# Kernel optimization log

Hardware: AMD Instinct MI355X
Metric: run time of the kernel (lower is better)

## Reference

```python
import jax, jax.numpy as jnp
import numpy as np

N_NODES = 50000
N_EDGES = 800000
NUM_FEATS = 128
HIDDEN = 256
NUM_GRAPHS = 512
BN_EPS = 1e-5


def setup_inputs() -> dict:
    key = jax.random.key(0)
    ks = jax.random.split(key, 12)
    x = jax.random.normal(ks[0], (N_NODES, NUM_FEATS), dtype=jnp.float32)
    edge_index = jax.random.randint(ks[1], (2, N_EDGES), 0, N_NODES, dtype=jnp.int64)
    batch = jnp.sort(jax.random.randint(ks[2], (N_NODES,), 0, NUM_GRAPHS, dtype=jnp.int64))
    s1 = 1.0 / np.sqrt(NUM_FEATS)
    s2 = 1.0 / np.sqrt(HIDDEN)
    return {
        "x": x,
        "edge_index": edge_index,
        "batch": batch,
        "w1a": jax.random.normal(ks[3], (NUM_FEATS, HIDDEN), dtype=jnp.float32) * s1,
        "b1a": jnp.zeros((HIDDEN,), jnp.float32),
        "w2a": jax.random.normal(ks[4], (HIDDEN, HIDDEN), dtype=jnp.float32) * s2,
        "b2a": jnp.zeros((HIDDEN,), jnp.float32),
        "ga": jnp.ones((HIDDEN,), jnp.float32),
        "ba": jnp.zeros((HIDDEN,), jnp.float32),
        "w1s": jax.random.normal(ks[5], (2, HIDDEN, HIDDEN), dtype=jnp.float32) * s2,
        "b1s": jnp.zeros((2, HIDDEN), jnp.float32),
        "w2s": jax.random.normal(ks[6], (2, HIDDEN, HIDDEN), dtype=jnp.float32) * s2,
        "b2s": jnp.zeros((2, HIDDEN), jnp.float32),
        "gs": jnp.ones((2, HIDDEN), jnp.float32),
        "bs": jnp.zeros((2, HIDDEN), jnp.float32),
    }


def _gin_layer(h, src, dst, w1, b1, w2, b2, gamma, beta):
    # GIN aggregation: (1 + eps=0) * x + sum over in-neighbors
    agg = jax.ops.segment_sum(h[src], dst, num_segments=N_NODES)
    z = h + agg
    z = jax.nn.relu(z @ w1 + b1)
    z = jax.nn.relu(z @ w2 + b2)
    # BatchNorm1d (training mode: biased batch statistics over nodes)
    mu = jnp.mean(z, axis=0)
    var = jnp.var(z, axis=0)
    return gamma * (z - mu) * jax.lax.rsqrt(var + BN_EPS) + beta


def reference(x, edge_index, batch, w1a, b1a, w2a, b2a, ga, ba,
              w1s, b1s, w2s, b2s, gs, bs):
    src, dst = edge_index[0], edge_index[1]
    h = _gin_layer(x, src, dst, w1a, b1a, w2a, b2a, ga, ba)
    for i in range(w1s.shape[0]):
        h = _gin_layer(h, src, dst, w1s[i], b1s[i], w2s[i], b2s[i], gs[i], bs[i])
    # global_mean_pool over graph ids
    sums = jax.ops.segment_sum(h, batch, num_segments=NUM_GRAPHS)
    counts = jax.ops.segment_sum(jnp.ones((h.shape[0],), h.dtype), batch,
                                 num_segments=NUM_GRAPHS)
    return sums / jnp.maximum(counts, 1.0)[:, None]
```

## Files before the change

kernel.cpp:

```cpp
#include <hip/hip_runtime.h>
#include <cstdint>
#include <cstddef>


constexpr int N_NODES  = 50000;
constexpr int N_EDGES  = 800000;
constexpr int F_IN     = 128;
constexpr int HID      = 256;
constexpr int N_GRAPHS = 512;
constexpr float BN_EPS = 1e-5f;

constexpr int SCAN_CHUNK = 4096;
constexpr int SCAN_NB    = (N_NODES + SCAN_CHUNK - 1) / SCAN_CHUNK;

typedef unsigned short u16;
typedef u16 u16x2 __attribute__((ext_vector_type(2)));
typedef u16 u16x4 __attribute__((ext_vector_type(4)));
typedef u16 u16x8 __attribute__((ext_vector_type(8)));
typedef __bf16 bf16x8 __attribute__((ext_vector_type(8)));
typedef float f32x4 __attribute__((ext_vector_type(4)));

__device__ __forceinline__ u16 f2bf(float f) {
    uint32_t u = __float_as_uint(f);
    uint32_t r = (u + 0x7FFFu + ((u >> 16) & 1u)) >> 16;
    return (u16)r;
}
__device__ __forceinline__ float bf2f(u16 h) {
    return __uint_as_float(((uint32_t)h) << 16);
}

__global__ void f2bf_k(const float* __restrict__ in, u16* __restrict__ outp, int n8) {
    int i = blockIdx.x * 256 + threadIdx.x;
    if (i >= n8) return;
    float4 a = reinterpret_cast<const float4*>(in)[i * 2];
    float4 b = reinterpret_cast<const float4*>(in)[i * 2 + 1];
    u16x8 v;
    v[0] = f2bf(a.x); v[1] = f2bf(a.y); v[2] = f2bf(a.z); v[3] = f2bf(a.w);
    v[4] = f2bf(b.x); v[5] = f2bf(b.y); v[6] = f2bf(b.z); v[7] = f2bf(b.w);
    reinterpret_cast<u16x8*>(outp)[i] = v;
}

__global__ void hist_k(const int* __restrict__ dst, int* __restrict__ deg) {
    int e = blockIdx.x * 256 + threadIdx.x;
    if (e < N_EDGES) atomicAdd(&deg[dst[e]], 1);
}

__global__ void scan_part1(const int* __restrict__ in, int* __restrict__ bsum) {
    __shared__ int sm[256];
    int t = threadIdx.x;
    int base = blockIdx.x * SCAN_CHUNK + t * 16;
    int s = 0;
#pragma unroll
    for (int j = 0; j < 16; j++) { int idx = base + j; s += (idx < N_NODES) ? in[idx] : 0; }
    sm[t] = s; __syncthreads();
    for (int off = 128; off > 0; off >>= 1) {
        if (t < off) sm[t] += sm[t + off];
        __syncthreads();
    }
    if (t == 0) bsum[blockIdx.x] = sm[0];
}

__global__ void scan_tops(int* __restrict__ bsum, int* __restrict__ rowptr) {
    if (threadIdx.x == 0 && blockIdx.x == 0) {
        int acc = 0;
        for (int i = 0; i < SCAN_NB; i++) { int v = bsum[i]; bsum[i] = acc; acc += v; }
        rowptr[N_NODES] = acc;
    }
}

__global__ void scan_final(const int* __restrict__ in, const int* __restrict__ bsum,
                           int* __restrict__ rowptr, int* __restrict__ cursor) {
    __shared__ int sm[256];
    int t = threadIdx.x;
    int base = blockIdx.x * SCAN_CHUNK + t * 16;
    int loc[16]; int s = 0;
#pragma unroll
    for (int j = 0; j < 16; j++) { int idx = base + j; loc[j] = s; s += (idx < N_NODES) ? in[idx] : 0; }
    sm[t] = s; __syncthreads();
    for (int off = 1; off < 256; off <<= 1) {
        int v = (t >= off) ? sm[t - off] : 0;
        __syncthreads();
        sm[t] += v;
        __syncthreads();
    }
    int excl = sm[t] - s + bsum[blockIdx.x];
#pragma unroll
    for (int j = 0; j < 16; j++) {
        int idx = base + j;
        if (idx < N_NODES) { int rp = excl + loc[j]; rowptr[idx] = rp; cursor[idx] = rp; }
    }
}

__global__ void build_csr(const int* __restrict__ src, const int* __restrict__ dst,
                          int* __restrict__ cursor, int* __restrict__ col) {
    int e = blockIdx.x * 256 + threadIdx.x;
    if (e < N_EDGES) {
        int d = dst[e];
        int p = atomicAdd(&cursor[d], 1);
        col[p] = src[e];
    }
}

template <int F, bool FOLD>
__global__ __launch_bounds__(256) void aggregate_k(const u16* __restrict__ h,
                                                   const int* __restrict__ rowptr,
                                                   const int* __restrict__ col,
                                                   const float* __restrict__ scsh,
                                                   u16* __restrict__ outp) {
    int node = blockIdx.x * 4 + (threadIdx.x >> 6);
    if (node >= N_NODES) return;
    int lane = threadIdx.x & 63;
    int beg = rowptr[node], end = rowptr[node + 1];
    if constexpr (F == 256) {
        const u16x4* hp = reinterpret_cast<const u16x4*>(h);
        u16x4 sv = hp[(size_t)node * 64 + lane];
        float acc[4] = {bf2f(sv[0]), bf2f(sv[1]), bf2f(sv[2]), bf2f(sv[3])};
        int e = beg;
        for (; e + 4 <= end; e += 4) {
            int s0 = col[e], s1 = col[e + 1], s2 = col[e + 2], s3 = col[e + 3];
            u16x4 v0 = hp[(size_t)s0 * 64 + lane];
            u16x4 v1 = hp[(size_t)s1 * 64 + lane];
            u16x4 v2 = hp[(size_t)s2 * 64 + lane];
            u16x4 v3 = hp[(size_t)s3 * 64 + lane];
#pragma unroll
            for (int i = 0; i < 4; i++)
                acc[i] += (bf2f(v0[i]) + bf2f(v1[i])) + (bf2f(v2[i]) + bf2f(v3[i]));
        }
        for (; e < end; ++e) {
            int s = col[e];
            u16x4 v = hp[(size_t)s * 64 + lane];
#pragma unroll
            for (int i = 0; i < 4; i++) acc[i] += bf2f(v[i]);
        }
        if constexpr (FOLD) {
            int c4 = lane * 4;
            float4 sc = *reinterpret_cast<const float4*>(&scsh[c4]);
            float4 sh = *reinterpret_cast<const float4*>(&scsh[HID + c4]);
            float m = (float)(end - beg + 1);
            acc[0] = acc[0] * sc.x + m * sh.x;
            acc[1] = acc[1] * sc.y + m * sh.y;
            acc[2] = acc[2] * sc.z + m * sh.z;
            acc[3] = acc[3] * sc.w + m * sh.w;
        }
        u16x4 r;
#pragma unroll
        for (int i = 0; i < 4; i++) r[i] = f2bf(acc[i]);
        reinterpret_cast<u16x4*>(outp)[(size_t)node * 64 + lane] = r;
    } else {
        const u16x2* hp = reinterpret_cast<const u16x2*>(h);
        u16x2 sv = hp[(size_t)node * 64 + lane];
        float acc[2] = {bf2f(sv[0]), bf2f(sv[1])};
        int e = beg;
        for (; e + 4 <= end; e += 4) {
            int s0 = col[e], s1 = col[e + 1], s2 = col[e + 2], s3 = col[e + 3];
            u16x2 v0 = hp[(size_t)s0 * 64 + lane];
            u16x2 v1 = hp[(size_t)s1 * 64 + lane];
            u16x2 v2 = hp[(size_t)s2 * 64 + lane];
            u16x2 v3 = hp[(size_t)s3 * 64 + lane];
#pragma unroll
            for (int i = 0; i < 2; i++)
                acc[i] += (bf2f(v0[i]) + bf2f(v1[i])) + (bf2f(v2[i]) + bf2f(v3[i]));
        }
        for (; e < end; ++e) {
            int s = col[e];
            u16x2 v = hp[(size_t)s * 64 + lane];
#pragma unroll
            for (int i = 0; i < 2; i++) acc[i] += bf2f(v[i]);
        }
        u16x2 r;
        r[0] = f2bf(acc[0]); r[1] = f2bf(acc[1]);
        reinterpret_cast<u16x2*>(outp)[(size_t)node * 64 + lane] = r;
    }
}

__global__ void wsplit_k(const float* __restrict__ W, u16* __restrict__ th,
                         u16* __restrict__ tl, int K) {
    int idx = blockIdx.x * 256 + threadIdx.x;
    int n = idx & 255, k = idx >> 8;
    float f = W[(size_t)k * 256 + n];
    u16 h = f2bf(f);
    th[(size_t)n * K + k] = h;
    tl[(size_t)n * K + k] = f2bf(f - bf2f(h));
}

template <int K, bool STATS>
__global__ __launch_bounds__(256, 2) void gemm_mfma(const u16* __restrict__ A,
                                                    const u16* __restrict__ Wth,
                                                    const u16* __restrict__ Wtl,
                                                    const float* __restrict__ bias,
                                                    u16* __restrict__ C,
                                                    float* __restrict__ stats) {
    constexpr int BM = 128, BK = 32;
    __shared__ alignas(16) u16 Ah[BM * BK];
    __shared__ alignas(16) u16 Bh[HID * BK];
    __shared__ alignas(16) u16 Bl[HID * BK];
    __shared__ float smsum[HID];
    __shared__ float smsq[HID];

    const int tid  = threadIdx.x;
    const int r0   = blockIdx.x * BM;
    const int lane = tid & 63, wid = tid >> 6;
    const int wm = wid >> 1, wn = wid & 1;
    const int l15 = lane & 15, kg = lane >> 4;

    const int arow = tid >> 1, ahalf = tid & 1;
    const bool avalid = (r0 + arow) < N_NODES;
    const u16* aptr = A + (size_t)(r0 + arow) * K + ahalf * 16;
    const u16* bhptr = Wth + (size_t)tid * K;
    const u16* blptr = Wtl + (size_t)tid * K;

    f32x4 acc[4][8];
#pragma unroll
    for (int i = 0; i < 4; i++)
#pragma unroll
        for (int j = 0; j < 8; j++) acc[i][j] = (f32x4){0.f, 0.f, 0.f, 0.f};

    for (int k0 = 0; k0 < K; k0 += BK) {
        u16x8 av[2];
        if (avalid) {
            av[0] = *reinterpret_cast<const u16x8*>(aptr + k0);
            av[1] = *reinterpret_cast<const u16x8*>(aptr + k0 + 8);
        } else {
            av[0] = (u16x8){0, 0, 0, 0, 0, 0, 0, 0};
            av[1] = av[0];
        }
#pragma unroll
        for (int j = 0; j < 2; j++) {
            int c = ahalf * 2 + j;
            int off = arow * 64 + ((c ^ ((arow >> 1) & 3)) << 4);
            *reinterpret_cast<u16x8*>((char*)Ah + off) = av[j];
        }
#pragma unroll
        for (int j = 0; j < 4; j++) {
            u16x8 v = *reinterpret_cast<const u16x8*>(bhptr + k0 + j * 8);
            int off = tid * 64 + ((j ^ ((tid >> 1) & 3)) << 4);
            *reinterpret_cast<u16x8*>((char*)Bh + off) = v;
        }
#pragma unroll
        for (int j = 0; j < 4; j++) {
            u16x8 v = *reinterpret_cast<const u16x8*>(blptr + k0 + j * 8);
            int off = tid * 64 + ((j ^ ((tid >> 1) & 3)) << 4);
            *reinterpret_cast<u16x8*>((char*)Bl + off) = v;
        }
        __syncthreads();
        bf16x8 ah[4];
#pragma unroll
        for (int mi = 0; mi < 4; mi++) {
            int r = wm * 64 + mi * 16 + l15;
            int off = r * 64 + ((kg ^ ((r >> 1) & 3)) << 4);
            ah[mi] = __builtin_bit_cast(bf16x8, *reinterpret_cast<const u16x8*>((const char*)Ah + off));
        }
#pragma unroll
        for (int ni = 0; ni < 8; ni++) {
            int n = wn * 128 + ni * 16 + l15;
            int off = n * 64 + ((kg ^ ((n >> 1) & 3)) << 4);
            bf16x8 bh = __builtin_bit_cast(bf16x8, *reinterpret_cast<const u16x8*>((const char*)Bh + off));
            bf16x8 bl = __builtin_bit_cast(bf16x8, *reinterpret_cast<const u16x8*>((const char*)Bl + off));
#pragma unroll
            for (int mi = 0; mi < 4; mi++) {
                acc[mi][ni] = __builtin_amdgcn_mfma_f32_16x16x32_bf16(ah[mi], bh, acc[mi][ni], 0, 0, 0);
                acc[mi][ni] = __builtin_amdgcn_mfma_f32_16x16x32_bf16(ah[mi], bl, acc[mi][ni], 0, 0, 0);
            }
        }
        __syncthreads();
    }
    if constexpr (STATS) {
        smsum[tid] = 0.f;
        smsq[tid]  = 0.f;
        __syncthreads();
    }
    float bv[8];
#pragma unroll
    for (int ni = 0; ni < 8; ni++) bv[ni] = bias[wn * 128 + ni * 16 + l15];
    float ps[8] = {}, pq[8] = {};
#pragma unroll
    for (int mi = 0; mi < 4; mi++) {
        int rowb = r0 + wm * 64 + mi * 16 + kg * 4;
#pragma unroll
        for (int rr = 0; rr < 4; rr++) {
            int row = rowb + rr;
            if (row < N_NODES) {
                u16* cp = C + (size_t)row * HID + wn * 128 + l15;
#pragma unroll
                for (int ni = 0; ni < 8; ni++) {
                    float v = fmaxf(acc[mi][ni][rr] + bv[ni], 0.f);
                    cp[ni * 16] = f2bf(v);
                    if constexpr (STATS) { ps[ni] += v; pq[ni] += v * v; }
                }
            }
        }
    }
    if constexpr (STATS) {
#pragma unroll
        for (int ni = 0; ni < 8; ni++) {
            int c = wn * 128 + ni * 16 + l15;
            atomicAdd(&smsum[c], ps[ni]);
            atomicAdd(&smsq[c], pq[ni]);
        }
        __syncthreads();
        atomicAdd(&stats[tid], smsum[tid]);
        atomicAdd(&stats[HID + tid], smsq[tid]);
    }
}

__global__ void bn_finalize(const float* __restrict__ stats, const float* __restrict__ gamma,
                            const float* __restrict__ beta, float* __restrict__ scsh) {
    int c = threadIdx.x;
    float mu  = stats[c] * (1.f / N_NODES);
    float var = stats[HID + c] * (1.f / N_NODES) - mu * mu;
    float g = gamma[c] * rsqrtf(var + BN_EPS);
    scsh[c] = g;
    scsh[HID + c] = beta[c] - mu * g;
}

__device__ __forceinline__ int lowerb(const int* a, int key) {
    int lo = 0, hi = N_NODES;
    while (lo < hi) { int mid = (lo + hi) >> 1; if (a[mid] < key) lo = mid + 1; else hi = mid; }
    return lo;
}

__global__ void pool_k(const u16* __restrict__ h, const int* __restrict__ batch,
                       const float* __restrict__ scsh, float* __restrict__ out) {
    __shared__ int bnd[2];
    int g = blockIdx.x;
    if (threadIdx.x == 0) bnd[0] = lowerb(batch, g);
    if (threadIdx.x == 1) bnd[1] = lowerb(batch, g + 1);
    __syncthreads();
    int lo = bnd[0], hi = bnd[1];
    int c = threadIdx.x;
    float s = 0.f;
    for (int r = lo; r < hi; ++r) s += bf2f(h[(size_t)r * HID + c]);
    int cnt = hi - lo;
    float v = (cnt > 0) ? (scsh[c] * (s / (float)cnt) + scsh[HID + c]) : 0.f;
    out[(size_t)g * HID + c] = v;
}

extern "C" void kernel_launch(void* const* d_in, const int* in_sizes, int n_in,
                              void* d_out, int out_size, void* d_ws, size_t ws_size,
                              hipStream_t stream) {
    const float* x   = (const float*)d_in[0];
    const int*   ei  = (const int*)d_in[1];
    const int* batch = (const int*)d_in[2];
    const float* w1a = (const float*)d_in[3];
    const float* b1a = (const float*)d_in[4];
    const float* w2a = (const float*)d_in[5];
    const float* b2a = (const float*)d_in[6];
    const float* ga  = (const float*)d_in[7];
    const float* ba  = (const float*)d_in[8];
    const float* w1s = (const float*)d_in[9];
    const float* b1s = (const float*)d_in[10];
    const float* w2s = (const float*)d_in[11];
    const float* b2s = (const float*)d_in[12];
    const float* gs  = (const float*)d_in[13];
    const float* bs  = (const float*)d_in[14];
    const int* src = ei;
    const int* dst = ei + N_EDGES;

    char* ws = (char*)d_ws;
    size_t off = 0;
    auto alloc = [&](size_t bytes) { void* p = ws + off; off += (bytes + 255) & ~(size_t)255; return p; };
    u16* A      = (u16*)alloc(sizeof(u16) * (size_t)N_NODES * HID);
    u16* B      = (u16*)alloc(sizeof(u16) * (size_t)N_NODES * HID);
    u16* Xb     = (u16*)alloc(sizeof(u16) * (size_t)N_NODES * F_IN);
    int* rowptr = (int*)alloc(sizeof(int) * (N_NODES + 1));
    int* deg    = (int*)alloc(sizeof(int) * N_NODES);
    int* cursor = (int*)alloc(sizeof(int) * N_NODES);
    int* col    = (int*)alloc(sizeof(int) * N_EDGES);
    int* bsum   = (int*)alloc(sizeof(int) * 64);
    float* stats  = (float*)alloc(sizeof(float) * 512 * 3);
    float* scsh   = (float*)alloc(sizeof(float) * 512 * 3);
    constexpr size_t WT_TOT = 32768 + 5 * 65536;
    u16* WtH = (u16*)alloc(sizeof(u16) * WT_TOT);
    u16* WtL = (u16*)alloc(sizeof(u16) * WT_TOT);
    constexpr size_t o1a = 0, o2a = 32768, o1s0 = 98304, o1s1 = 163840, o2s0 = 229376, o2s1 = 294912;
    float* out    = (float*)d_out;
    (void)ws_size; (void)in_sizes; (void)n_in; (void)out_size;

    f2bf_k<<<(N_NODES * F_IN / 8 + 255) / 256, 256, 0, stream>>>(x, Xb, N_NODES * F_IN / 8);
    wsplit_k<<<128, 256, 0, stream>>>(w1a,          WtH + o1a,  WtL + o1a,  128);
    wsplit_k<<<256, 256, 0, stream>>>(w2a,          WtH + o2a,  WtL + o2a,  256);
    wsplit_k<<<256, 256, 0, stream>>>(w1s,          WtH + o1s0, WtL + o1s0, 256);
    wsplit_k<<<256, 256, 0, stream>>>(w1s + 65536,  WtH + o1s1, WtL + o1s1, 256);
    wsplit_k<<<256, 256, 0, stream>>>(w2s,          WtH + o2s0, WtL + o2s0, 256);
    wsplit_k<<<256, 256, 0, stream>>>(w2s + 65536,  WtH + o2s1, WtL + o2s1, 256);
    hipMemsetAsync(stats, 0, sizeof(float) * 512 * 3, stream);

    hipMemsetAsync(deg, 0, sizeof(int) * N_NODES, stream);
    hist_k<<<N_EDGES / 256, 256, 0, stream>>>(dst, deg);
    scan_part1<<<SCAN_NB, 256, 0, stream>>>(deg, bsum);
    scan_tops<<<1, 64, 0, stream>>>(bsum, rowptr);
    scan_final<<<SCAN_NB, 256, 0, stream>>>(deg, bsum, rowptr, cursor);
    build_csr<<<N_EDGES / 256, 256, 0, stream>>>(src, dst, cursor, col);

    const int AGG_GRID  = (N_NODES + 3) / 4;
    const int GEMM_GRID = (N_NODES + 127) / 128;

    aggregate_k<128, false><<<AGG_GRID, 256, 0, stream>>>(Xb, rowptr, col, nullptr, A);
    gemm_mfma<128, false><<<GEMM_GRID, 256, 0, stream>>>(A, WtH + o1a, WtL + o1a, b1a, B, nullptr);
    gemm_mfma<256, true><<<GEMM_GRID, 256, 0, stream>>>(B, WtH + o2a, WtL + o2a, b2a, B, stats);
    bn_finalize<<<1, 256, 0, stream>>>(stats, ga, ba, scsh);

    aggregate_k<256, true><<<AGG_GRID, 256, 0, stream>>>(B, rowptr, col, scsh, A);
    gemm_mfma<256, false><<<GEMM_GRID, 256, 0, stream>>>(A, WtH + o1s0, WtL + o1s0, b1s, A, nullptr);
    gemm_mfma<256, true><<<GEMM_GRID, 256, 0, stream>>>(A, WtH + o2s0, WtL + o2s0, b2s, A, stats + 512);
    bn_finalize<<<1, 256, 0, stream>>>(stats + 512, gs, bs, scsh + 512);

    aggregate_k<256, true><<<AGG_GRID, 256, 0, stream>>>(A, rowptr, col, scsh + 512, B);
    gemm_mfma<256, false><<<GEMM_GRID, 256, 0, stream>>>(B, WtH + o1s1, WtL + o1s1, b1s + 256, B, nullptr);
    gemm_mfma<256, true><<<GEMM_GRID, 256, 0, stream>>>(B, WtH + o2s1, WtL + o2s1, b2s + 256, B, stats + 1024);
    bn_finalize<<<1, 256, 0, stream>>>(stats + 1024, gs + 256, bs + 256, scsh + 1024);

    pool_k<<<N_GRAPHS, 256, 0, stream>>>(B, batch, scsh + 1024, out);
}
```

Before: 497.5 us.

## Load GEMM tiles directly to LDS and fold BN finalize into consumers

```diff
diff --git a/kernel.cpp b/kernel.cpp
--- a/kernel.cpp
+++ b/kernel.cpp
@@ -27,6 +27,12 @@
 }
 __device__ __forceinline__ float bf2f(u16 h) {
     return __uint_as_float(((uint32_t)h) << 16);
+}
+
+__device__ __forceinline__ void gload16(const void* g, void* l) {
+    __builtin_amdgcn_global_load_lds(
+        (const __attribute__((address_space(1))) uint32_t*)g,
+        (__attribute__((address_space(3))) uint32_t*)l, 16, 0, 0);
 }
 
 __global__ void f2bf_k(const float* __restrict__ in, u16* __restrict__ outp, int n8) {
@@ -105,13 +111,27 @@
 __global__ __launch_bounds__(256) void aggregate_k(const u16* __restrict__ h,
                                                    const int* __restrict__ rowptr,
                                                    const int* __restrict__ col,
-                                                   const float* __restrict__ scsh,
+                                                   const float* __restrict__ stats,
+                                                   const float* __restrict__ gamma,
+                                                   const float* __restrict__ beta,
                                                    u16* __restrict__ outp) {
     int node = blockIdx.x * 4 + (threadIdx.x >> 6);
     if (node >= N_NODES) return;
     int lane = threadIdx.x & 63;
     int beg = rowptr[node], end = rowptr[node + 1];
     if constexpr (F == 256) {
+        float sc[4], sh[4];
+        if constexpr (FOLD) {
+            int c4 = lane * 4;
+#pragma unroll
+            for (int i = 0; i < 4; i++) {
+                float mu  = stats[c4 + i] * (1.f / N_NODES);
+                float var = stats[HID + c4 + i] * (1.f / N_NODES) - mu * mu;
+                float g = gamma[c4 + i] * rsqrtf(var + BN_EPS);
+                sc[i] = g;
+                sh[i] = beta[c4 + i] - mu * g;
+            }
+        }
         const u16x4* hp = reinterpret_cast<const u16x4*>(h);
         u16x4 sv = hp[(size_t)node * 64 + lane];
         float acc[4] = {bf2f(sv[0]), bf2f(sv[1]), bf2f(sv[2]), bf2f(sv[3])};
@@ -133,14 +153,9 @@
             for (int i = 0; i < 4; i++) acc[i] += bf2f(v[i]);
         }
         if constexpr (FOLD) {
-            int c4 = lane * 4;
-            float4 sc = *reinterpret_cast<const float4*>(&scsh[c4]);
-            float4 sh = *reinterpret_cast<const float4*>(&scsh[HID + c4]);
             float m = (float)(end - beg + 1);
-            acc[0] = acc[0] * sc.x + m * sh.x;
-            acc[1] = acc[1] * sc.y + m * sh.y;
-            acc[2] = acc[2] * sc.z + m * sh.z;
-            acc[3] = acc[3] * sc.w + m * sh.w;
+#pragma unroll
+            for (int i = 0; i < 4; i++) acc[i] = acc[i] * sc[i] + m * sh[i];
         }
         u16x4 r;
 #pragma unroll
@@ -173,14 +188,26 @@
     }
 }
 
-__global__ void wsplit_k(const float* __restrict__ W, u16* __restrict__ th,
-                         u16* __restrict__ tl, int K) {
+__global__ void wsplit_all(const float* __restrict__ w1a, const float* __restrict__ w2a,
+                           const float* __restrict__ w1s, const float* __restrict__ w2s,
+                           u16* __restrict__ th, u16* __restrict__ tl) {
     int idx = blockIdx.x * 256 + threadIdx.x;
-    int n = idx & 255, k = idx >> 8;
+    const float* W; int local; size_t dof;
+    if (idx < 32768)       { W = w1a;         local = idx;          dof = 0; }
+    else if (idx < 98304)  { W = w2a;         local = idx - 32768;  dof = 32768; }
+    else if (idx < 163840) { W = w1s;         local = idx - 98304;  dof = 98304; }
+    else if (idx < 229376) { W = w1s + 65536; local = idx - 163840; dof = 163840; }
+    else if (idx < 294912) { W = w2s;         local = idx - 229376; dof = 229376; }
+    else if (idx < 360448) { W = w2s + 65536; local = idx - 294912; dof = 294912; }
+    else return;
+    int n = local & 255, k = local >> 8;
     float f = W[(size_t)k * 256 + n];
     u16 h = f2bf(f);
-    th[(size_t)n * K + k] = h;
-    tl[(size_t)n * K + k] = f2bf(f - bf2f(h));
+    int t = k >> 5, j = (k >> 3) & 3, e = k & 7;
+    int uo = j ^ ((n >> 1) & 3);
+    size_t di = dof + (size_t)t * 8192 + n * 32 + uo * 8 + e;
+    th[di] = h;
+    tl[di] = f2bf(f - bf2f(h));
 }
 
 template <int K, bool STATS>
@@ -199,15 +226,19 @@
 
     const int tid  = threadIdx.x;
     const int r0   = blockIdx.x * BM;
-    const int lane = tid & 63, wid = tid >> 6;
-    const int wm = wid >> 1, wn = wid & 1;
+    const int lane = tid & 63, wv = tid >> 6;
+    const int wm = wv >> 1, wn = wv & 1;
     const int l15 = lane & 15, kg = lane >> 4;
 
-    const int arow = tid >> 1, ahalf = tid & 1;
-    const bool avalid = (r0 + arow) < N_NODES;
-    const u16* aptr = A + (size_t)(r0 + arow) * K + ahalf * 16;
-    const u16* bhptr = Wth + (size_t)tid * K;
-    const u16* blptr = Wtl + (size_t)tid * K;
+    int aro[2], aco[2];
+#pragma unroll
+    for (int p = 0; p < 2; p++) {
+        int nu = wv * 128 + p * 64 + lane;
+        int r = nu >> 2, us = nu & 3;
+        int u = us ^ ((r >> 1) & 3);
+        aro[p] = r;
+        aco[p] = u * 8;
+    }
 
     f32x4 acc[4][8];
 #pragma unroll
@@ -216,31 +247,18 @@
         for (int j = 0; j < 8; j++) acc[i][j] = (f32x4){0.f, 0.f, 0.f, 0.f};
 
     for (int k0 = 0; k0 < K; k0 += BK) {
-        u16x8 av[2];
-        if (avalid) {
-            av[0] = *reinterpret_cast<const u16x8*>(aptr + k0);
-            av[1] = *reinterpret_cast<const u16x8*>(aptr + k0 + 8);
-        } else {
-            av[0] = (u16x8){0, 0, 0, 0, 0, 0, 0, 0};
-            av[1] = av[0];
-        }
-#pragma unroll
-        for (int j = 0; j < 2; j++) {
-            int c = ahalf * 2 + j;
-            int off = arow * 64 + ((c ^ ((arow >> 1) & 3)) << 4);
-            *reinterpret_cast<u16x8*>((char*)Ah + off) = av[j];
-        }
-#pragma unroll
-        for (int j = 0; j < 4; j++) {
-            u16x8 v = *reinterpret_cast<const u16x8*>(bhptr + k0 + j * 8);
-            int off = tid * 64 + ((j ^ ((tid >> 1) & 3)) << 4);
-            *reinterpret_cast<u16x8*>((char*)Bh + off) = v;
-        }
-#pragma unroll
-        for (int j = 0; j < 4; j++) {
-            u16x8 v = *reinterpret_cast<const u16x8*>(blptr + k0 + j * 8);
-            int off = tid * 64 + ((j ^ ((tid >> 1) & 3)) << 4);
-            *reinterpret_cast<u16x8*>((char*)Bl + off) = v;
+        int t = k0 >> 5;
+#pragma unroll
+        for (int p = 0; p < 2; p++) {
+            const u16* src = A + (size_t)(r0 + aro[p]) * K + k0 + aco[p];
+            gload16(src, (char*)Ah + (size_t)(wv * 2 + p) * 1024);
+        }
+        const char* wh = (const char*)Wth + (size_t)t * 16384 + (size_t)wv * 4096 + (size_t)lane * 16;
+        const char* wl = (const char*)Wtl + (size_t)t * 16384 + (size_t)wv * 4096 + (size_t)lane * 16;
+#pragma unroll
+        for (int c = 0; c < 4; c++) {
+            gload16(wh + c * 1024, (char*)Bh + (size_t)wv * 4096 + c * 1024);
+            gload16(wl + c * 1024, (char*)Bl + (size_t)wv * 4096 + c * 1024);
         }
         __syncthreads();
         bf16x8 ah[4];
@@ -303,16 +321,6 @@
     }
 }
 
-__global__ void bn_finalize(const float* __restrict__ stats, const float* __restrict__ gamma,
-                            const float* __restrict__ beta, float* __restrict__ scsh) {
-    int c = threadIdx.x;
-    float mu  = stats[c] * (1.f / N_NODES);
-    float var = stats[HID + c] * (1.f / N_NODES) - mu * mu;
-    float g = gamma[c] * rsqrtf(var + BN_EPS);
-    scsh[c] = g;
-    scsh[HID + c] = beta[c] - mu * g;
-}
-
 __device__ __forceinline__ int lowerb(const int* a, int key) {
     int lo = 0, hi = N_NODES;
     while (lo < hi) { int mid = (lo + hi) >> 1; if (a[mid] < key) lo = mid + 1; else hi = mid; }
@@ -320,7 +328,8 @@
 }
 
 __global__ void pool_k(const u16* __restrict__ h, const int* __restrict__ batch,
-                       const float* __restrict__ scsh, float* __restrict__ out) {
+                       const float* __restrict__ stats, const float* __restrict__ gamma,
+                       const float* __restrict__ beta, float* __restrict__ out) {
     __shared__ int bnd[2];
     int g = blockIdx.x;
     if (threadIdx.x == 0) bnd[0] = lowerb(batch, g);
@@ -328,10 +337,14 @@
     __syncthreads();
     int lo = bnd[0], hi = bnd[1];
     int c = threadIdx.x;
+    float mu  = stats[c] * (1.f / N_NODES);
+    float var = stats[HID + c] * (1.f / N_NODES) - mu * mu;
+    float sc = gamma[c] * rsqrtf(var + BN_EPS);
+    float sh = beta[c] - mu * sc;
     float s = 0.f;
     for (int r = lo; r < hi; ++r) s += bf2f(h[(size_t)r * HID + c]);
     int cnt = hi - lo;
-    float v = (cnt > 0) ? (scsh[c] * (s / (float)cnt) + scsh[HID + c]) : 0.f;
+    float v = (cnt > 0) ? (sc * (s / (float)cnt) + sh) : 0.f;
     out[(size_t)g * HID + c] = v;
 }
 
@@ -368,7 +381,6 @@
     int* col    = (int*)alloc(sizeof(int) * N_EDGES);
     int* bsum   = (int*)alloc(sizeof(int) * 64);
     float* stats  = (float*)alloc(sizeof(float) * 512 * 3);
-    float* scsh   = (float*)alloc(sizeof(float) * 512 * 3);
     constexpr size_t WT_TOT = 32768 + 5 * 65536;
     u16* WtH = (u16*)alloc(sizeof(u16) * WT_TOT);
     u16* WtL = (u16*)alloc(sizeof(u16) * WT_TOT);
@@ -377,12 +389,7 @@
     (void)ws_size; (void)in_sizes; (void)n_in; (void)out_size;
 
     f2bf_k<<<(N_NODES * F_IN / 8 + 255) / 256, 256, 0, stream>>>(x, Xb, N_NODES * F_IN / 8);
-    wsplit_k<<<128, 256, 0, stream>>>(w1a,          WtH + o1a,  WtL + o1a,  128);
-    wsplit_k<<<256, 256, 0, stream>>>(w2a,          WtH + o2a,  WtL + o2a,  256);
-    wsplit_k<<<256, 256, 0, stream>>>(w1s,          WtH + o1s0, WtL + o1s0, 256);
-    wsplit_k<<<256, 256, 0, stream>>>(w1s + 65536,  WtH + o1s1, WtL + o1s1, 256);
-    wsplit_k<<<256, 256, 0, stream>>>(w2s,          WtH + o2s0, WtL + o2s0, 256);
-    wsplit_k<<<256, 256, 0, stream>>>(w2s + 65536,  WtH + o2s1, WtL + o2s1, 256);
+    wsplit_all<<<(360448 + 255) / 256, 256, 0, stream>>>(w1a, w2a, w1s, w2s, WtH, WtL);
     hipMemsetAsync(stats, 0, sizeof(float) * 512 * 3, stream);
 
     hipMemsetAsync(deg, 0, sizeof(int) * N_NODES, stream);
@@ -395,20 +402,17 @@
     const int AGG_GRID  = (N_NODES + 3) / 4;
     const int GEMM_GRID = (N_NODES + 127) / 128;
 
-    aggregate_k<128, false><<<AGG_GRID, 256, 0, stream>>>(Xb, rowptr, col, nullptr, A);
+    aggregate_k<128, false><<<AGG_GRID, 256, 0, stream>>>(Xb, rowptr, col, nullptr, nullptr, nullptr, A);
     gemm_mfma<128, false><<<GEMM_GRID, 256, 0, stream>>>(A, WtH + o1a, WtL + o1a, b1a, B, nullptr);
     gemm_mfma<256, true><<<GEMM_GRID, 256, 0, stream>>>(B, WtH + o2a, WtL + o2a, b2a, B, stats);
-    bn_finalize<<<1, 256, 0, stream>>>(stats, ga, ba, scsh);
-
-    aggregate_k<256, true><<<AGG_GRID, 256, 0, stream>>>(B, rowptr, col, scsh, A);
+
+    aggregate_k<256, true><<<AGG_GRID, 256, 0, stream>>>(B, rowptr, col, stats, ga, ba, A);
     gemm_mfma<256, false><<<GEMM_GRID, 256, 0, stream>>>(A, WtH + o1s0, WtL + o1s0, b1s, A, nullptr);
     gemm_mfma<256, true><<<GEMM_GRID, 256, 0, stream>>>(A, WtH + o2s0, WtL + o2s0, b2s, A, stats + 512);
-    bn_finalize<<<1, 256, 0, stream>>>(stats + 512, gs, bs, scsh + 512);
-
-    aggregate_k<256, true><<<AGG_GRID, 256, 0, stream>>>(A, rowptr, col, scsh + 512, B);
+
+    aggregate_k<256, true><<<AGG_GRID, 256, 0, stream>>>(A, rowptr, col, stats + 512, gs, bs, B);
     gemm_mfma<256, false><<<GEMM_GRID, 256, 0, stream>>>(B, WtH + o1s1, WtL + o1s1, b1s + 256, B, nullptr);
     gemm_mfma<256, true><<<GEMM_GRID, 256, 0, stream>>>(B, WtH + o2s1, WtL + o2s1, b2s + 256, B, stats + 1024);
-    bn_finalize<<<1, 256, 0, stream>>>(stats + 1024, gs + 256, bs + 256, scsh + 1024);
-
-    pool_k<<<N_GRAPHS, 256, 0, stream>>>(B, batch, scsh + 1024, out);
-}
+
+    pool_k<<<N_GRAPHS, 256, 0, stream>>>(B, batch, stats + 1024, gs + 256, bs + 256, out);
+}
```

Result: faster. 461.0 us, median of 2 (-7.3%).
